# Performance work log

Hardware: AMD Instinct MI355X
Metric: run time of the kernel (lower is better)

## Reference

```python
import jax, jax.numpy as jnp
import numpy as np

IN_DIM, COND_DIM, OUT_DIM = 256, 256, 128
B, LQ, LK = 4, 4096, 4096


def setup_inputs() -> dict:
    key = jax.random.key(0)
    ks = jax.random.split(key, 8)
    s_in = 1.0 / np.sqrt(IN_DIM)
    s_c = 1.0 / np.sqrt(COND_DIM)
    return {
        "x": jax.random.normal(ks[0], (B, LQ, IN_DIM), dtype=jnp.float32),
        "cond": jax.random.normal(ks[1], (B, LK, COND_DIM), dtype=jnp.float32),
        "Wq": jax.random.uniform(ks[2], (IN_DIM, OUT_DIM), jnp.float32, -s_in, s_in),
        "bq": jax.random.uniform(ks[3], (OUT_DIM,), jnp.float32, -s_in, s_in),
        "Wk": jax.random.uniform(ks[4], (COND_DIM, OUT_DIM), jnp.float32, -s_c, s_c),
        "bk": jax.random.uniform(ks[5], (OUT_DIM,), jnp.float32, -s_c, s_c),
        "Wv": jax.random.uniform(ks[6], (COND_DIM, OUT_DIM), jnp.float32, -s_c, s_c),
        "bv": jax.random.uniform(ks[7], (OUT_DIM,), jnp.float32, -s_c, s_c),
    }


def reference(x, cond, Wq, bq, Wk, bk, Wv, bv):
    # q: [B, Lq, D], k/v: [B, Lk, D]
    q = jnp.einsum("bqi,id->bqd", x, Wq) + bq
    k = jnp.einsum("bkc,cd->bkd", cond, Wk) + bk
    v = jnp.einsum("bkc,cd->bkd", cond, Wv) + bv
    # NOTE: original uses UNscaled dot product (no 1/sqrt(d)).
    scores = jnp.einsum("bqd,bkd->bqk", q, k)  # [B, Lq, Lk]
    attn = jax.nn.softmax(scores, axis=-1)
    return jnp.einsum("bqk,bkd->bqd", attn, v)  # [B, Lq, D]
```

## Files before the change

kernel.cpp:

```cpp
#include <hip/hip_runtime.h>
#include <hip/hip_bf16.h>


typedef __attribute__((ext_vector_type(8))) short short8;
typedef __attribute__((ext_vector_type(8))) unsigned short ushort8;
typedef __attribute__((ext_vector_type(4))) unsigned short us4;
typedef __attribute__((ext_vector_type(4))) float f32x4;
typedef __attribute__((ext_vector_type(16))) float f32x16;
typedef __attribute__((ext_vector_type(4))) unsigned int u32x4;
typedef __bf16 bf16x8 __attribute__((ext_vector_type(8)));

constexpr int BATCH  = 4;
constexpr int SEQLEN = 4096;
constexpr int DIN    = 256;
constexpr int DOUT   = 128;
constexpr int ROWS   = BATCH * SEQLEN;
constexpr float LOG2E = 1.4426950408889634f;

static __device__ __forceinline__ unsigned short bf16_rn(float f) {
  unsigned int u = __builtin_bit_cast(unsigned int, f);
  unsigned int r = u + 0x7FFFu + ((u >> 16) & 1u);
  return (unsigned short)(r >> 16);
}
static __device__ __forceinline__ float bf16_f32(unsigned short h) {
  return __builtin_bit_cast(float, (unsigned int)h << 16);
}

static __device__ __forceinline__ f32x4 mfma_bf16(short8 a, short8 b, f32x4 c) {
  return __builtin_amdgcn_mfma_f32_16x16x32_bf16(
      __builtin_bit_cast(bf16x8, a), __builtin_bit_cast(bf16x8, b), c, 0, 0, 0);
}
static __device__ __forceinline__ f32x16 mfma32(short8 a, short8 b, f32x16 c) {
  return __builtin_amdgcn_mfma_f32_32x32x16_bf16(
      __builtin_bit_cast(bf16x8, a), __builtin_bit_cast(bf16x8, b), c, 0, 0, 0);
}

static __device__ __forceinline__ unsigned int cvt_pk(float lo, float hi) {
  unsigned int r;
  asm("v_cvt_pk_bf16_f32 %0, %1, %2" : "=v"(r) : "v"(lo), "v"(hi));
  return r;
}
static __device__ __forceinline__ void permswap(unsigned int& a, unsigned int& b) {
  asm("v_permlane32_swap_b32 %0, %1" : "+v"(a), "+v"(b));
}

static __device__ __forceinline__ int swz128(int a) {
  return a ^ (((a >> 7) & 7) << 4);
}
static __device__ __forceinline__ int swzK(int a) {
  return a ^ (((a >> 8) & 15) << 4);
}


__global__ __launch_bounds__(256) void proj_kernel(
    const float* __restrict__ x, const float* __restrict__ cond,
    const float* __restrict__ Wq, const float* __restrict__ bq,
    const float* __restrict__ Wk, const float* __restrict__ bk,
    const float* __restrict__ Wv, const float* __restrict__ bv,
    unsigned short* __restrict__ qb, unsigned short* __restrict__ kb,
    unsigned short* __restrict__ vt)
{
  const int which = blockIdx.y;
  const float* __restrict__ src  = (which == 0) ? x  : cond;
  const float* __restrict__ W    = (which == 0) ? Wq : (which == 1 ? Wk : Wv);
  const float* __restrict__ bias = (which == 0) ? bq : (which == 1 ? bk : bv);
  const int r0 = blockIdx.x * 64;

  __shared__ __align__(16) char lds[32768];
  char* const AhB = lds;
  char* const AlB = lds + 8192;
  char* const WtB = lds + 16384;

  const int tid  = threadIdx.x;
  const int wv   = tid >> 6;
  const int lane = tid & 63;
  const int g    = lane >> 4;
  const int c    = lane & 15;

  f32x4 acc[8];
  #pragma unroll
  for (int cf = 0; cf < 8; ++cf) acc[cf] = (f32x4){0.f, 0.f, 0.f, 0.f};

  for (int kt = 0; kt < 4; ++kt) {
    #pragma unroll
    for (int i = 0; i < 4; ++i) {
      const int idx = tid + i * 256;
      const int row = idx >> 4, f4 = idx & 15;
      const float4 a4 =
          *(const float4*)(src + (size_t)(r0 + row) * DIN + kt * 64 + f4 * 4);
      us4 hi, lo;
      const float av[4] = {a4.x, a4.y, a4.z, a4.w};
      #pragma unroll
      for (int e = 0; e < 4; ++e) {
        hi[e] = bf16_rn(av[e]);
        lo[e] = bf16_rn(av[e] - bf16_f32(hi[e]));
      }
      const int off = swz128(row * 128 + f4 * 8);
      *(us4*)(AhB + off) = hi;
      *(us4*)(AlB + off) = lo;
    }
    {
      const int col = tid & 127, half = tid >> 7;
      #pragma unroll
      for (int j = 0; j < 4; ++j) {
        const int k0 = half * 32 + j * 8;
        ushort8 wb;
        #pragma unroll
        for (int e = 0; e < 8; ++e)
          wb[e] = bf16_rn(W[(size_t)(kt * 64 + k0 + e) * DOUT + col]);
        *(ushort8*)(WtB + swz128(col * 128 + k0 * 2)) = wb;
      }
    }
    __syncthreads();

    #pragma unroll
    for (int ks = 0; ks < 2; ++ks) {
      const int aoff = (wv * 16 + c) * 128 + ks * 64 + g * 16;
      const short8 ah = *(const short8*)(AhB + swz128(aoff));
      const short8 al = *(const short8*)(AlB + swz128(aoff));
      #pragma unroll
      for (int cf = 0; cf < 8; ++cf) {
        const short8 wb =
            *(const short8*)(WtB + swz128((cf * 16 + c) * 128 + ks * 64 + g * 16));
        acc[cf] = mfma_bf16(ah, wb, acc[cf]);
        acc[cf] = mfma_bf16(al, wb, acc[cf]);
      }
    }
    __syncthreads();
  }

  if (which == 0) {
    #pragma unroll
    for (int cf = 0; cf < 8; ++cf) {
      const float bb = bias[cf * 16 + c];
      #pragma unroll
      for (int r = 0; r < 4; ++r)
        qb[(size_t)(r0 + wv * 16 + g * 4 + r) * DOUT + cf * 16 + c] =
            bf16_rn((acc[cf][r] + bb) * LOG2E);
    }
  } else if (which == 1) {
    char* const Ktile = lds;
    #pragma unroll
    for (int cf = 0; cf < 8; ++cf) {
      const float bb = bias[cf * 16 + c];
      #pragma unroll
      for (int r = 0; r < 4; ++r) {
        const int row = wv * 16 + g * 4 + r;
        *(unsigned short*)(Ktile + swzK(row * 256 + (cf * 16 + c) * 2)) =
            bf16_rn(acc[cf][r] + bb);
      }
    }
    __syncthreads();
    const int b2     = r0 >> 12;
    const int kblkG0 = (r0 & 4095) >> 5;
    #pragma unroll
    for (int j = 0; j < 4; ++j) {
      const int i    = tid + j * 256;
      const int kblk = i >> 9;
      const int rem  = i & 511;
      const int f    = rem >> 6;
      const int ln   = rem & 63;
      const int row  = kblk * 32 + (ln & 31);
      const int colb = f * 32 + (ln >> 5) * 16;
      const ushort8 v = *(const ushort8*)(Ktile + swzK(row * 256 + colb));
      *(ushort8*)((char*)kb +
          (((size_t)(b2 * 128 + kblkG0 + kblk) * 8 + f) * 64 + ln) * 16) = v;
    }
  } else {
    const int keybase = r0 + wv * 16 + g * 4;
    const int b2   = keybase >> 12;
    const int kblk = (keybase & 4095) >> 5;
    const int kk   = (keybase >> 4) & 1;
    const int h    = (keybase >> 3) & 1;
    const int e0   = keybase & 7;
    #pragma unroll
    for (int cf = 0; cf < 8; ++cf) {
      const float bb = bias[cf * 16 + c];
      const int col  = cf * 16 + c;
      const int dblk = col >> 5, l31 = col & 31;
      us4 pk;
      #pragma unroll
      for (int r = 0; r < 4; ++r) pk[r] = bf16_rn(acc[cf][r] + bb);
      *(us4*)(vt + (((((size_t)b2 * 128 + kblk) * 4 + dblk) * 2 + kk) * 64 +
                    h * 32 + l31) * 8 + e0) = pk;
    }
  }
}

constexpr int NSPLIT = 4;
constexpr int QBLK   = 32;
constexpr int KVBLK  = 32;
constexpr int ITERS  = SEQLEN / NSPLIT / KVBLK;

__global__ __launch_bounds__(256, 2) void attn_kernel(
    const unsigned short* __restrict__ qb,
    const unsigned short* __restrict__ kb,
    const unsigned short* __restrict__ vt,
    float* __restrict__ out)
{
  __shared__ __align__(16) float cmb[2][32][132];
  __shared__ float Ml[NSPLIT][32][2];

  const int bid = ((blockIdx.x & 7) << 6) | (blockIdx.x >> 3);
  const int qt  = bid & 127;
  const int b   = bid >> 7;
  const int tid = threadIdx.x;
  const int split = tid >> 6;
  const int lane  = tid & 63;
  const int ql = lane & 31;
  const int h  = lane >> 5;

  const int q0 = qt * QBLK;

  short8 qf[8];
  {
    const char* qp = (const char*)(qb + (size_t)(b * SEQLEN + q0 + ql) * DOUT) + h * 16;
    #pragma unroll
    for (int f = 0; f < 8; ++f) qf[f] = *(const short8*)(qp + f * 32);
  }

  const int kblk0 = split * (SEQLEN / NSPLIT / 32);
  const char* kfb = (const char*)kb + ((size_t)b * 128 + kblk0) * 8192 + lane * 16;
  const char* vfb = (const char*)vt + ((size_t)b * 128 + kblk0) * 8192 + lane * 16;

  f32x16 acc[4];
  #pragma unroll
  for (int d = 0; d < 4; ++d)
    #pragma unroll
    for (int r = 0; r < 16; ++r) acc[d][r] = 0.f;
  float mc = -1e30f, lc = 0.f;

  short8 kf[8], vf[4][2];
  #pragma unroll
  for (int f = 0; f < 8; ++f) kf[f] = *(const short8*)(kfb + f * 1024);
  #pragma unroll
  for (int d = 0; d < 4; ++d)
    #pragma unroll
    for (int kk = 0; kk < 2; ++kk)
      vf[d][kk] = *(const short8*)(vfb + (d * 2 + kk) * 1024);

  for (int t = 0; t < ITERS; ++t) {
    const bool more = (t + 1 < ITERS);

    f32x16 s;
    #pragma unroll
    for (int r = 0; r < 16; ++r) s[r] = 0.f;
    __builtin_amdgcn_s_setprio(1);
    #pragma unroll
    for (int f = 0; f < 8; ++f) s = mfma32(kf[f], qf[f], s);
    __builtin_amdgcn_s_setprio(0);

    if (more) {
      kfb += 8192;
      #pragma unroll
      for (int f = 0; f < 8; ++f) kf[f] = *(const short8*)(kfb + f * 1024);
    }

    float m01 = fmaxf(fmaxf(s[0],  s[1]),  s[2]);
    float m02 = fmaxf(fmaxf(s[3],  s[4]),  s[5]);
    float m03 = fmaxf(fmaxf(s[6],  s[7]),  s[8]);
    float m04 = fmaxf(fmaxf(s[9],  s[10]), s[11]);
    float m05 = fmaxf(fmaxf(s[12], s[13]), s[14]);
    float m11 = fmaxf(fmaxf(m01, m02), m03);
    float m12 = fmaxf(fmaxf(m04, m05), s[15]);
    float tm  = fmaxf(m11, m12);
    if (!__all(tm <= mc + 8.f)) {
      float tr = fmaxf(tm, __shfl_xor(tm, 32));
      const float mnew  = fmaxf(mc, tr);
      const float sc    = exp2f(mc - mnew);
      mc = mnew;
      lc *= sc;
      #pragma unroll
      for (int d = 0; d < 4; ++d)
        #pragma unroll
        for (int r = 0; r < 16; ++r) acc[d][r] *= sc;
    }
    float p[16];
    float rs = 0.f;
    #pragma unroll
    for (int r = 0; r < 16; ++r) {
      p[r] = exp2f(s[r] - mc);
      rs += p[r];
    }
    lc += rs;

    short8 pfrag[2];
    #pragma unroll
    for (int kk = 0; kk < 2; ++kk) {
      unsigned int A  = cvt_pk(p[kk * 8 + 0], p[kk * 8 + 1]);
      unsigned int Bv = cvt_pk(p[kk * 8 + 2], p[kk * 8 + 3]);
      unsigned int C  = cvt_pk(p[kk * 8 + 4], p[kk * 8 + 5]);
      unsigned int Dv = cvt_pk(p[kk * 8 + 6], p[kk * 8 + 7]);
      permswap(A, C);
      permswap(Bv, Dv);
      const u32x4 w = {A, Bv, C, Dv};
      pfrag[kk] = __builtin_bit_cast(short8, w);
    }

    __builtin_amdgcn_s_setprio(1);
    #pragma unroll
    for (int d = 0; d < 4; ++d)
      #pragma unroll
      for (int kk = 0; kk < 2; ++kk)
        acc[d] = mfma32(vf[d][kk], pfrag[kk], acc[d]);
    __builtin_amdgcn_s_setprio(0);

    if (more) {
      vfb += 8192;
      #pragma unroll
      for (int d = 0; d < 4; ++d)
        #pragma unroll
        for (int kk = 0; kk < 2; ++kk)
          vf[d][kk] = *(const short8*)(vfb + (d * 2 + kk) * 1024);
    }
  }

  lc += __shfl_xor(lc, 32);
  if (lane < 32) { Ml[split][ql][0] = mc; Ml[split][ql][1] = lc; }
  __syncthreads();

  float mg = -1e30f, lsum = 0.f;
  #pragma unroll
  for (int s2 = 0; s2 < NSPLIT; ++s2) mg = fmaxf(mg, Ml[s2][ql][0]);
  #pragma unroll
  for (int s2 = 0; s2 < NSPLIT; ++s2)
    lsum += Ml[s2][ql][1] * exp2f(Ml[s2][ql][0] - mg);
  const float fac = exp2f(mc - mg);
  #pragma unroll
  for (int d = 0; d < 4; ++d)
    #pragma unroll
    for (int r = 0; r < 16; ++r) acc[d][r] *= fac;

  if (split & 1) {
    float* reg = &cmb[split >> 1][0][0];
    #pragma unroll
    for (int d = 0; d < 4; ++d)
      #pragma unroll
      for (int rr = 0; rr < 4; ++rr) {
        const f32x4 v = {acc[d][rr*4+0], acc[d][rr*4+1], acc[d][rr*4+2], acc[d][rr*4+3]};
        *(f32x4*)(reg + ql * 132 + d * 32 + rr * 8 + h * 4) = v;
      }
  }
  __syncthreads();
  if (!(split & 1)) {
    const float* reg = &cmb[split >> 1][0][0];
    #pragma unroll
    for (int d = 0; d < 4; ++d)
      #pragma unroll
      for (int rr = 0; rr < 4; ++rr) {
        const f32x4 v = *(const f32x4*)(reg + ql * 132 + d * 32 + rr * 8 + h * 4);
        acc[d][rr*4+0] += v.x; acc[d][rr*4+1] += v.y;
        acc[d][rr*4+2] += v.z; acc[d][rr*4+3] += v.w;
      }
  }
  __syncthreads();
  if (split == 2) {
    float* reg = &cmb[0][0][0];
    #pragma unroll
    for (int d = 0; d < 4; ++d)
      #pragma unroll
      for (int rr = 0; rr < 4; ++rr) {
        const f32x4 v = {acc[d][rr*4+0], acc[d][rr*4+1], acc[d][rr*4+2], acc[d][rr*4+3]};
        *(f32x4*)(reg + ql * 132 + d * 32 + rr * 8 + h * 4) = v;
      }
  }
  __syncthreads();
  if (split == 0) {
    const float* reg = &cmb[0][0][0];
    const float inv = 1.f / lsum;
    float* const op = out + (size_t)(b * SEQLEN + q0 + ql) * DOUT;
    #pragma unroll
    for (int d = 0; d < 4; ++d)
      #pragma unroll
      for (int rr = 0; rr < 4; ++rr) {
        const f32x4 v = *(const f32x4*)(reg + ql * 132 + d * 32 + rr * 8 + h * 4);
        f32x4 o;
        o.x = (acc[d][rr*4+0] + v.x) * inv;
        o.y = (acc[d][rr*4+1] + v.y) * inv;
        o.z = (acc[d][rr*4+2] + v.z) * inv;
        o.w = (acc[d][rr*4+3] + v.w) * inv;
        *(f32x4*)(op + d * 32 + rr * 8 + h * 4) = o;
      }
  }
}

extern "C" void kernel_launch(void* const* d_in, const int* in_sizes, int n_in,
                              void* d_out, int out_size, void* d_ws, size_t ws_size,
                              hipStream_t stream) {
  const float* x    = (const float*)d_in[0];
  const float* cond = (const float*)d_in[1];
  const float* Wq   = (const float*)d_in[2];
  const float* bq   = (const float*)d_in[3];
  const float* Wk   = (const float*)d_in[4];
  const float* bk   = (const float*)d_in[5];
  const float* Wv   = (const float*)d_in[6];
  const float* bv   = (const float*)d_in[7];
  float* out = (float*)d_out;

  unsigned short* qb = (unsigned short*)d_ws;
  unsigned short* kb = qb + (size_t)ROWS * DOUT;
  unsigned short* vt = kb + (size_t)ROWS * DOUT;

  proj_kernel<<<dim3(ROWS / 64, 3), 256, 0, stream>>>(
      x, cond, Wq, bq, Wk, bk, Wv, bv, qb, kb, vt);

  attn_kernel<<<dim3(BATCH * (SEQLEN / QBLK)), 256, 0, stream>>>(
      qb, kb, vt, out);
}
```

Before: 74.57 us.

## Double-buffer K fragments, split QK accumulation chains, use native exp2

K fragments are now double-buffered in two register sets, so each K tile is prefetched two iterations ahead. The loop is unrolled by two via a lambda. The QK^T MFMA chain is split into two independent accumulators that are summed afterwards, which shortens the dependency chain. exp2f is replaced with the raw hardware exp2 builtin, the row sum uses a tree reduction, and the lazy-rescale threshold is raised from 8 to 11. Costs are higher register pressure from the extra K buffer and accumulator, an assumption that ITERS is even, and a larger unnormalised exponent range before rescaling.

```diff
diff --git a/kernel.cpp b/kernel.cpp
--- a/kernel.cpp
+++ b/kernel.cpp
@@ -24,6 +24,9 @@
 }
 static __device__ __forceinline__ float bf16_f32(unsigned short h) {
   return __builtin_bit_cast(float, (unsigned int)h << 16);
+}
+static __device__ __forceinline__ float exp2n(float x) {
+  return __builtin_amdgcn_exp2f(x);
 }
 
 static __device__ __forceinline__ f32x4 mfma_bf16(short8 a, short8 b, f32x4 c) {
@@ -230,31 +233,38 @@
     for (int r = 0; r < 16; ++r) acc[d][r] = 0.f;
   float mc = -1e30f, lc = 0.f;
 
-  short8 kf[8], vf[4][2];
-  #pragma unroll
-  for (int f = 0; f < 8; ++f) kf[f] = *(const short8*)(kfb + f * 1024);
+  short8 kfA[8], kfB[8], vf[4][2];
+  #pragma unroll
+  for (int f = 0; f < 8; ++f) kfA[f] = *(const short8*)(kfb + f * 1024);
+  #pragma unroll
+  for (int f = 0; f < 8; ++f) kfB[f] = *(const short8*)(kfb + 8192 + f * 1024);
+  kfb += 16384;
   #pragma unroll
   for (int d = 0; d < 4; ++d)
     #pragma unroll
     for (int kk = 0; kk < 2; ++kk)
       vf[d][kk] = *(const short8*)(vfb + (d * 2 + kk) * 1024);
 
-  for (int t = 0; t < ITERS; ++t) {
-    const bool more = (t + 1 < ITERS);
-
-    f32x16 s;
-    #pragma unroll
-    for (int r = 0; r < 16; ++r) s[r] = 0.f;
+  auto body = [&](short8 (&kf)[8], int t) {
+    f32x16 s0, s1;
+    #pragma unroll
+    for (int r = 0; r < 16; ++r) { s0[r] = 0.f; s1[r] = 0.f; }
     __builtin_amdgcn_s_setprio(1);
     #pragma unroll
-    for (int f = 0; f < 8; ++f) s = mfma32(kf[f], qf[f], s);
+    for (int f = 0; f < 4; ++f) s0 = mfma32(kf[f], qf[f], s0);
+    #pragma unroll
+    for (int f = 0; f < 4; ++f) s1 = mfma32(kf[f + 4], qf[f + 4], s1);
     __builtin_amdgcn_s_setprio(0);
 
-    if (more) {
+    if (t + 2 < ITERS) {
+      #pragma unroll
+      for (int f = 0; f < 8; ++f) kf[f] = *(const short8*)(kfb + f * 1024);
       kfb += 8192;
-      #pragma unroll
-      for (int f = 0; f < 8; ++f) kf[f] = *(const short8*)(kfb + f * 1024);
-    }
+    }
+
+    float s[16];
+    #pragma unroll
+    for (int r = 0; r < 16; ++r) s[r] = s0[r] + s1[r];
 
     float m01 = fmaxf(fmaxf(s[0],  s[1]),  s[2]);
     float m02 = fmaxf(fmaxf(s[3],  s[4]),  s[5]);
@@ -264,10 +274,10 @@
     float m11 = fmaxf(fmaxf(m01, m02), m03);
     float m12 = fmaxf(fmaxf(m04, m05), s[15]);
     float tm  = fmaxf(m11, m12);
-    if (!__all(tm <= mc + 8.f)) {
+    if (!__all(tm <= mc + 11.f)) {
       float tr = fmaxf(tm, __shfl_xor(tm, 32));
       const float mnew  = fmaxf(mc, tr);
-      const float sc    = exp2f(mc - mnew);
+      const float sc    = exp2n(mc - mnew);
       mc = mnew;
       lc *= sc;
       #pragma unroll
@@ -276,13 +286,13 @@
         for (int r = 0; r < 16; ++r) acc[d][r] *= sc;
     }
     float p[16];
-    float rs = 0.f;
-    #pragma unroll
-    for (int r = 0; r < 16; ++r) {
-      p[r] = exp2f(s[r] - mc);
-      rs += p[r];
-    }
-    lc += rs;
+    #pragma unroll
+    for (int r = 0; r < 16; ++r) p[r] = exp2n(s[r] - mc);
+    float a0 = (p[0]+p[1]) + (p[2]+p[3]);
+    float a1 = (p[4]+p[5]) + (p[6]+p[7]);
+    float a2 = (p[8]+p[9]) + (p[10]+p[11]);
+    float a3 = (p[12]+p[13]) + (p[14]+p[15]);
+    lc += (a0 + a1) + (a2 + a3);
 
     short8 pfrag[2];
     #pragma unroll
@@ -305,7 +315,7 @@
         acc[d] = mfma32(vf[d][kk], pfrag[kk], acc[d]);
     __builtin_amdgcn_s_setprio(0);
 
-    if (more) {
+    if (t + 1 < ITERS) {
       vfb += 8192;
       #pragma unroll
       for (int d = 0; d < 4; ++d)
@@ -313,6 +323,11 @@
         for (int kk = 0; kk < 2; ++kk)
           vf[d][kk] = *(const short8*)(vfb + (d * 2 + kk) * 1024);
     }
+  };
+
+  for (int t = 0; t < ITERS; t += 2) {
+    body(kfA, t);
+    body(kfB, t + 1);
   }
 
   lc += __shfl_xor(lc, 32);
@@ -324,8 +339,8 @@
   for (int s2 = 0; s2 < NSPLIT; ++s2) mg = fmaxf(mg, Ml[s2][ql][0]);
   #pragma unroll
   for (int s2 = 0; s2 < NSPLIT; ++s2)
-    lsum += Ml[s2][ql][1] * exp2f(Ml[s2][ql][0] - mg);
-  const float fac = exp2f(mc - mg);
+    lsum += Ml[s2][ql][1] * exp2n(Ml[s2][ql][0] - mg);
+  const float fac = exp2n(mc - mg);
   #pragma unroll
   for (int d = 0; d < 4; ++d)
     #pragma unroll
```

Result: faster. 71.42 us, median of 3 (-4.2%).
